# Optimization experiments

Measured on AMD Instinct MI355X. Metric: run time of the kernel, lower is better.

The kernel has to match this reference:

```python
import jax, jax.numpy as jnp
import numpy as np

EPS = 1e-5   # torch F.layer_norm default eps
TOP_K = 20   # int(3*D^2 / (2*hr*N^2 + 10*D)) for D=768, N=196, hr=1.0
NUM_EXPERTS = 200  # 10 * TOP_K


def setup_inputs() -> dict:
    key = jax.random.key(0)
    ks = jax.random.split(key, 6)
    B, N, D = 32, 196, 768
    E, H = NUM_EXPERTS, 196  # H = int(N * hidden_ratio)
    s = 0.02
    return {
        "x": jax.random.normal(ks[0], (B, N, D), jnp.float32),
        "Wr": jax.random.normal(ks[1], (E, D), jnp.float32) * s,   # router.weight
        "W1": jax.random.normal(ks[2], (E, H, N), jnp.float32) * s,  # fc1.weight per expert
        "b1": jnp.zeros((E, H), jnp.float32),
        "W2": jax.random.normal(ks[3], (E, N, H), jnp.float32) * s,  # fc2.weight per expert
        "b2": jnp.zeros((E, N), jnp.float32),
        "Wo": jax.random.normal(ks[4], (D, D), jnp.float32) * s,     # out_proj.weight
        "bo": jnp.zeros((D,), jnp.float32),
    }


def reference(x, Wr, W1, b1, W2, b2, Wo, bo):
    B, N, D = x.shape
    E = Wr.shape[0]
    K = TOP_K

    # Router: per-sample routing on token-mean features
    logits = x.mean(axis=1) @ Wr.T                      # (B, E)
    probs = jax.nn.softmax(logits, axis=-1)             # (B, E)
    w, idx = jax.lax.top_k(probs, K)                    # (B, K) sorted desc, as torch.topk
    w = w / w.sum(axis=-1, keepdims=True)               # renormalize top-k weights

    # TokenMixer operates in (B, D, N) space: layernorm over tokens (no affine),
    # then fc1 (N->H), gelu(tanh), fc2 (H->N).
    xt = jnp.swapaxes(x, 1, 2)                          # (B, D, N)
    mu = xt.mean(axis=-1, keepdims=True)
    var = xt.var(axis=-1, keepdims=True)                # population var (matches F.layer_norm)
    z = (xt - mu) * jax.lax.rsqrt(var + EPS)            # (B, D, N)

    # Gather each sample's K expert weight matrices and batch the MLPs.
    W1g, b1g = W1[idx], b1[idx]                         # (B,K,H,N), (B,K,H)
    W2g, b2g = W2[idx], b2[idx]                         # (B,K,N,H), (B,K,N)

    h = jnp.einsum('bdn,bkhn->bkdh', z, W1g) + b1g[:, :, None, :]
    a = jax.nn.gelu(h, approximate=True)                # tanh-approx GELU
    o = jnp.einsum('bkdh,bknh->bkdn', a, W2g) + b2g[:, :, None, :]

    # Weighted combine over the K selected experts, back to (B, N, D)
    mix = jnp.einsum('bk,bkdn->bnd', w, o)

    out = mix @ Wo.T + bo                               # out_proj

    # Load-balancing aux loss (top-1 assignment fraction vs mean router prob)
    top1 = jax.nn.one_hot(idx[:, 0], E, dtype=probs.dtype)   # (B, E)
    aux = E * jnp.sum(probs.mean(axis=0) * top1.mean(axis=0))
    return out, aux
```

## Files before the change

kernel.cpp:

```cpp
#include <hip/hip_runtime.h>
#include <math.h>

constexpr int B  = 32;
constexpr int N  = 196;
constexpr int D  = 768;
constexpr int E  = 200;
constexpr int TK = 20;

constexpr int NGRP = 4;
constexpr int PRB  = 14336;
constexpr int EXB  = 114688;
constexpr int LK   = 40;

typedef __bf16 bf16x8 __attribute__((ext_vector_type(8)));
typedef __bf16 bf16x4 __attribute__((ext_vector_type(4)));
typedef float  f32x4  __attribute__((ext_vector_type(4)));
typedef long   longx2 __attribute__((ext_vector_type(2)));
typedef unsigned char uchar;

#define GLDS16(gp, lp)                                                        \
  __builtin_amdgcn_global_load_lds(                                           \
      (const __attribute__((address_space(1))) void*)(gp),                    \
      (__attribute__((address_space(3))) void*)(lp), 16, 0, 0)

#define WAITVM12  __builtin_amdgcn_s_waitcnt(0x0F7C)
#define WAITVM8   __builtin_amdgcn_s_waitcnt(0x0F78)
#define WAITVM0   __builtin_amdgcn_s_waitcnt(0x0F70)
#define WAITLGKM0 __builtin_amdgcn_s_waitcnt(0xC07F)
#define BAR       __builtin_amdgcn_s_barrier()

#define KEEP64(v) asm volatile("" : : "v"(v))

__device__ __forceinline__ float gelu_fast(float x) {
  float u = x * fmaf(x * x, 0.044715f, 1.0f);
  float e = exp2f(-2.3022084f * u);
  return x * __builtin_amdgcn_rcpf(1.0f + e);
}

__device__ __forceinline__ uchar f32_to_f8(float v) {
  return (uchar)(__builtin_amdgcn_cvt_pk_fp8_f32(v, v, 0, false) & 0xff);
}

__global__ __launch_bounds__(256) void k_ln(const float* __restrict__ x,
                                            uchar* __restrict__ zb,
                                            float* __restrict__ mu) {
  int b = blockIdx.x / 12, dt = blockIdx.x % 12;
  int d0 = dt * 64;
  int t = threadIdx.x;
  int q = t >> 6, d = t & 63;
  __shared__ float ps[256], pq[256];
  __shared__ float ms[64], rss[64];
  __shared__ alignas(16) uchar zt[64 * 256];

  for (int i = t; i < 1024; i += 256) ((uint4*)zt)[i] = (uint4){0, 0, 0, 0};

  const float* xp = x + ((size_t)b * N + q * 49) * D + d0 + d;
  float v[49];
  float s = 0.f, sq = 0.f;
  #pragma unroll
  for (int n = 0; n < 49; ++n) {
    v[n] = xp[(size_t)n * D];
    s += v[n]; sq += v[n] * v[n];
  }
  ps[t] = s; pq[t] = sq;
  __syncthreads();
  if (t < 64) {
    float S = ps[t] + ps[t + 64] + ps[t + 128] + ps[t + 192];
    float Q = pq[t] + pq[t + 64] + pq[t + 128] + pq[t + 192];
    float m = S * (1.0f / N);
    float var = Q * (1.0f / N) - m * m;
    ms[t] = m; rss[t] = rsqrtf(var + 1e-5f);
    mu[(size_t)b * D + d0 + t] = m;
  }
  __syncthreads();
  float m = ms[d], r = rss[d];
  int dsw = (d >> 1) & 3;
  #pragma unroll
  for (int n = 0; n < 49; ++n) {
    int tok = q * 49 + n;
    int qp = ((tok >> 3) & 3) ^ dsw;
    int off = d * 256 + (tok >> 6) * 64 + qp * 16 + ((tok >> 5) & 1) * 8 + (tok & 7);
    zt[off] = f32_to_f8((v[n] - m) * r);
  }
  __syncthreads();
  #pragma unroll
  for (int pair = 0; pair < 4; ++pair) {
    uint4* dst = (uint4*)(zb + (((size_t)b * 4 + pair) * 768 + d0) * 64);
    dst[t] = ((const uint4*)zt)[(t >> 2) * 16 + pair * 4 + (t & 3)];
  }
}

__global__ __launch_bounds__(256) void k_prep(
    const float* __restrict__ W1, const float* __restrict__ W2,
    const float* __restrict__ Wo,
    uchar* __restrict__ Wf, __bf16* __restrict__ Wob,
    const float* __restrict__ mu, const float* __restrict__ Wr,
    float* __restrict__ probs, int* __restrict__ idxg,
    float* __restrict__ wg) {
  int bx = blockIdx.x;
  int t = threadIdx.x;
  __shared__ alignas(16) uchar ls[112 * 256];
  __shared__ float sp[E];
  __shared__ float smax, ssum;
  __shared__ float svals[TK];
  __shared__ int   sidx[TK];

  if (bx >= 1376) {
    int b = bx - 1376;
    int lane = t & 63, wave = t >> 6;
    float* smu = (float*)ls;
    for (int i = t; i < 768; i += 256) smu[i] = mu[(size_t)b * D + i];
    __syncthreads();
    const float4* m4 = (const float4*)smu;
    #pragma unroll 1
    for (int i = 0; i < 50; ++i) {
      int e = wave * 50 + i;
      const float4* wr4 = (const float4*)(Wr + (size_t)e * D);
      float acc = 0.f;
      #pragma unroll
      for (int j = 0; j < 3; ++j) {
        float4 w = wr4[lane + j * 64], mm = m4[lane + j * 64];
        acc = fmaf(w.x, mm.x, acc); acc = fmaf(w.y, mm.y, acc);
        acc = fmaf(w.z, mm.z, acc); acc = fmaf(w.w, mm.w, acc);
      }
      #pragma unroll
      for (int off = 32; off > 0; off >>= 1) acc += __shfl_down(acc, off);
      if (lane == 0) sp[e] = acc;
    }
    __syncthreads();
    if (t < 64) {
      float mx = -1e30f;
      for (int e = t; e < E; e += 64) mx = fmaxf(mx, sp[e]);
      #pragma unroll
      for (int off = 32; off > 0; off >>= 1) mx = fmaxf(mx, __shfl_down(mx, off));
      if (t == 0) smax = mx;
    }
    __syncthreads();
    if (t < E) sp[t] = exp2f((sp[t] - smax) * 1.44269504f);
    __syncthreads();
    if (t < 64) {
      float s = 0.f;
      for (int e = t; e < E; e += 64) s += sp[e];
      #pragma unroll
      for (int off = 32; off > 0; off >>= 1) s += __shfl_down(s, off);
      if (t == 0) ssum = s;
    }
    __syncthreads();
    if (t < E) {
      sp[t] = sp[t] / ssum;
      probs[(size_t)b * E + t] = sp[t];
    }
    __syncthreads();
    for (int k = 0; k < TK; ++k) {
      if (t < 64) {
        float bv = -1e30f; int bi = 0;
        for (int e = t; e < E; e += 64) {
          float v = sp[e];
          if (v > bv) { bv = v; bi = e; }
        }
        #pragma unroll
        for (int off = 32; off > 0; off >>= 1) {
          float ov = __shfl_down(bv, off);
          int   oi = __shfl_down(bi, off);
          if (ov > bv || (ov == bv && oi < bi)) { bv = ov; bi = oi; }
        }
        if (t == 0) {
          svals[k] = bv; sidx[k] = bi;
          sp[bi] = -2e30f;
        }
      }
      __syncthreads();
    }
    if (t == 0) {
      float s = 0.f;
      for (int k = 0; k < TK; ++k) s += svals[k];
      float inv = 1.0f / s;
      for (int k = 0; k < TK; ++k) {
        wg[b * TK + k]   = svals[k] * inv;
        idxg[b * TK + k] = sidx[k];
      }
    }
    return;
  }

  if (bx >= 800) {
    int i = (bx - 800) * 256 + t;
    float4 v = *(const float4*)&Wo[(size_t)i * 4];
    bf16x4 o = {(__bf16)v.x, (__bf16)v.y, (__bf16)v.z, (__bf16)v.w};
    *(bf16x4*)&Wob[(size_t)i * 4] = o;
    return;
  }

  int e = bx >> 2, mat = (bx >> 1) & 1, half = bx & 1;
  int r0 = half * 112;
  int nrows = half ? 84 : 112;
  for (int i = t; i < 1792; i += 256) ((uint4*)ls)[i] = (uint4){0, 0, 0, 0};
  __syncthreads();
  const float* src = (mat ? W2 : W1) + (size_t)e * 196 * 196;
  for (int i = t; i < nrows * 49; i += 256) {
    int rl = i / 49, c4 = (i - rl * 49) * 4;
    float4 v = *(const float4*)&src[(size_t)(r0 + rl) * 196 + c4];
    int lo = __builtin_amdgcn_cvt_pk_fp8_f32(v.x, v.y, 0, false);
    unsigned int pk = (unsigned int)__builtin_amdgcn_cvt_pk_fp8_f32(v.z, v.w, lo, true);
    *(unsigned int*)&ls[rl * 256 + c4] = pk;
  }
  __syncthreads();
  uchar* dst = Wf + (size_t)e * EXB + mat * 4 * PRB;
  for (int s = t; s < 1792; s += 256) {
    int p = s / 448, rem = s - p * 448;
    int cl = rem >> 2, qp = rem & 3;
    int col = r0 + cl;
    int ql = qp ^ ((col >> 1) & 3);
    unsigned long lo = *(const unsigned long*)&ls[cl * 256 + p * 64 + ql * 8];
    unsigned long hi = *(const unsigned long*)&ls[cl * 256 + p * 64 + 32 + ql * 8];
    longx2 o; o[0] = (long)lo; o[1] = (long)hi;
    *(longx2*)&dst[(size_t)(p * 896 + col * 4 + qp) * 16] = o;
  }
}

__global__ __launch_bounds__(256, 2) void k_expert(
    const uchar* __restrict__ zb, const uchar* __restrict__ Wf,
    const float* __restrict__ b1, const float* __restrict__ b2,
    const int* __restrict__ idxg, const float* __restrict__ wg,
    __bf16* __restrict__ mixg) {
  __shared__ alignas(16) uchar pool[75776];
  __shared__ alignas(16) __bf16 b1s[5 * 196];
  __shared__ float bsum_s[196];
  __shared__ int   eidx_s[5];
  __shared__ float w_s[5];
  uchar* zs  = pool;
  uchar* at  = pool + 16384;
  uchar* wsb = pool + 32768;
  __bf16* tb = (__bf16*)pool;

  int xw = blockIdx.x & 7, rr_ = blockIdx.x >> 3;
  int j = rr_ / 12, dt = rr_ - j * 12;
  int gid = j * 8 + xw;
  int g = gid & 3, b = gid >> 2;
  int d0 = dt * 64;

  int t = threadIdx.x;
  int lane = t & 63, wave = t >> 6;
  int quad = lane >> 4, l16 = lane & 15;
  int wrow = (wave & 1) * 32;
  int wcol = (wave >> 1) * 112;
  int qp = quad ^ ((l16 >> 1) & 3);

  if (t < 5) {
    eidx_s[t] = idxg[b * TK + g * 5 + t];
    w_s[t]    = wg[b * TK + g * 5 + t];
  }
  for (int i = t; i < 980; i += 256) {
    int kk = i / 196, col = i - kk * 196;
    int ee = idxg[b * TK + g * 5 + kk];
    b1s[i] = (__bf16)b1[ee * 196 + col];
  }
  if (t < 196) {
    float s = 0.f;
    #pragma unroll
    for (int k5 = 0; k5 < 5; ++k5) {
      int ee = idxg[b * TK + g * 5 + k5];
      s += wg[b * TK + g * 5 + k5] * b2[ee * 196 + t];
    }
    bsum_s[t] = s;
  }
  __syncthreads();

  {
    const uchar* zbase = zb + ((size_t)b * 4 * 768 + d0) * 64;
    #pragma unroll
    for (int p = 0; p < 4; ++p)
      GLDS16(zbase + (size_t)p * (768 * 64) + t * 16, zs + p * 4096 + t * 16);
  }

  int s0 = t * 16, s1 = (t + 256) * 16, s2 = (t + 512) * 16;
  int s3 = ((t & 127) + 768) * 16;

  auto issue = [&](int qn) {
    int qq = qn > 39 ? 39 : qn;
    int kk2 = qq >> 3, rem = qq & 7;
    const uchar* src = Wf + (size_t)eidx_s[kk2] * EXB + rem * PRB;
    int bi = qn & 3;
    uchar* lb = (bi == 3) ? pool : wsb + bi * PRB;
    GLDS16(src + s0, lb + s0);
    GLDS16(src + s1, lb + s1);
    GLDS16(src + s2, lb + s2);
    GLDS16(src + s3, lb + s3);
  };
  issue(0); issue(1); issue(2);

  WAITVM12;
  BAR;
  const uchar* zbase_l = zs + (wrow + l16) * 64 + qp * 16;
  longx2 zf[3][2];
  #pragma unroll
  for (int p = 0; p < 3; ++p) {
    zf[p][0] = *(const longx2*)(zbase_l + p * 4096);
    zf[p][1] = *(const longx2*)(zbase_l + p * 4096 + 1024);
  }
  long z3r0, z3r1;
  {
    longx2 zt0 = *(const longx2*)(zbase_l + 3 * 4096);
    longx2 zt1 = *(const longx2*)(zbase_l + 3 * 4096 + 1024);
    KEEP64(zt0[1]); KEEP64(zt1[1]);
    z3r0 = zt0[0]; z3r1 = zt1[0];
  }

  const uchar* abase = at + (wrow + l16) * 64 + qp * 16;

  f32x4 macc[14];
  #pragma unroll
  for (int i = 0; i < 14; ++i) macc[i] = (f32x4){0.f, 0.f, 0.f, 0.f};

  #pragma unroll 1
  for (int kk = 0; kk < 5; ++kk) {
    float wkv = w_s[kk];
    f32x4 hacc[14];
    #pragma unroll
    for (int i = 0; i < 14; ++i) hacc[i] = (f32x4){0.f, 0.f, 0.f, 0.f};

    #pragma unroll 1
    for (int p = 0; p < 3; ++p) {
      int q = kk * 8 + p;
      WAITVM8;
      BAR;
      int bi = q & 3;
      const uchar* buf = (bi == 3) ? pool : wsb + bi * PRB;
      const uchar* bb = buf + (wcol + l16) * 64 + qp * 16;
      __builtin_amdgcn_s_setprio(1);
      #pragma unroll
      for (int ct = 0; ct < 7; ++ct) {
        longx2 bf = *(const longx2*)(bb + ct * 1024);
        hacc[ct]     = __builtin_amdgcn_mfma_f32_16x16x32_fp8_fp8(bf[0], zf[p][0][0], hacc[ct], 0, 0, 0);
        hacc[ct]     = __builtin_amdgcn_mfma_f32_16x16x32_fp8_fp8(bf[1], zf[p][0][1], hacc[ct], 0, 0, 0);
        hacc[7 + ct] = __builtin_amdgcn_mfma_f32_16x16x32_fp8_fp8(bf[0], zf[p][1][0], hacc[7 + ct], 0, 0, 0);
        hacc[7 + ct] = __builtin_amdgcn_mfma_f32_16x16x32_fp8_fp8(bf[1], zf[p][1][1], hacc[7 + ct], 0, 0, 0);
      }
      __builtin_amdgcn_s_setprio(0);
      issue(q + 3);
    }
    {
      int q = kk * 8 + 3;
      WAITVM8;
      BAR;
      int bi = q & 3;
      const uchar* buf = (bi == 3) ? pool : wsb + bi * PRB;
      const uchar* bb = buf + (wcol + l16) * 64 + qp * 16;
      __builtin_amdgcn_s_setprio(1);
      #pragma unroll
      for (int ct = 0; ct < 7; ++ct) {
        longx2 bf = *(const longx2*)(bb + ct * 1024);
        KEEP64(bf[1]);
        hacc[ct]     = __builtin_amdgcn_mfma_f32_16x16x32_fp8_fp8(bf[0], z3r0, hacc[ct], 0, 0, 0);
        hacc[7 + ct] = __builtin_amdgcn_mfma_f32_16x16x32_fp8_fp8(bf[0], z3r1, hacc[7 + ct], 0, 0, 0);
      }
      __builtin_amdgcn_s_setprio(0);
      issue(q + 3);
    }

    #pragma unroll
    for (int ct = 0; ct < 7; ++ct) {
      int hb = wcol + ct * 16 + quad * 4;
      bool valid = hb < 196;
      unsigned pk0 = 0u, pk1 = 0u;
      if (valid) {
        bf16x4 b4 = *(const bf16x4*)&b1s[kk * 196 + hb];
        float bv0 = (float)b4[0], bv1 = (float)b4[1];
        float bv2 = (float)b4[2], bv3 = (float)b4[3];
        f32x4 h0 = hacc[ct], h1 = hacc[7 + ct];
        pk0 = (unsigned)__builtin_amdgcn_cvt_pk_fp8_f32(
                  gelu_fast(h0[0] + bv0) * wkv, gelu_fast(h0[1] + bv1) * wkv, 0, false);
        pk0 = (unsigned)__builtin_amdgcn_cvt_pk_fp8_f32(
                  gelu_fast(h0[2] + bv2) * wkv, gelu_fast(h0[3] + bv3) * wkv, (int)pk0, true);
        pk1 = (unsigned)__builtin_amdgcn_cvt_pk_fp8_f32(
                  gelu_fast(h1[0] + bv0) * wkv, gelu_fast(h1[1] + bv1) * wkv, 0, false);
        pk1 = (unsigned)__builtin_amdgcn_cvt_pk_fp8_f32(
                  gelu_fast(h1[2] + bv2) * wkv, gelu_fast(h1[3] + bv3) * wkv, (int)pk1, true);
      }
      int d0r = wrow + l16;
      int addr0 = (hb >> 6) * 4096 + d0r * 64 + ((((hb >> 3) & 3) ^ ((d0r >> 1) & 3)) << 4)
                + ((hb >> 5) & 1) * 8 + (quad & 1) * 4;
      *(unsigned*)&at[addr0]        = pk0;
      *(unsigned*)&at[addr0 + 1024] = pk1;
    }
    WAITLGKM0;

    #pragma unroll 1
    for (int p = 0; p < 3; ++p) {
      int q = kk * 8 + 4 + p;
      WAITVM8;
      BAR;
      int bi = q & 3;
      const uchar* buf = (bi == 3) ? pool : wsb + bi * PRB;
      const uchar* bb = buf + (wcol + l16) * 64 + qp * 16;
      longx2 a0 = *(const longx2*)(abase + p * 4096);
      longx2 a1 = *(const longx2*)(abase + p * 4096 + 1024);
      __builtin_amdgcn_s_setprio(1);
      #pragma unroll
      for (int ct = 0; ct < 7; ++ct) {
        longx2 bf = *(const longx2*)(bb + ct * 1024);
        macc[ct]     = __builtin_amdgcn_mfma_f32_16x16x32_fp8_fp8(a0[0], bf[0], macc[ct], 0, 0, 0);
        macc[ct]     = __builtin_amdgcn_mfma_f32_16x16x32_fp8_fp8(a0[1], bf[1], macc[ct], 0, 0, 0);
        macc[7 + ct] = __builtin_amdgcn_mfma_f32_16x16x32_fp8_fp8(a1[0], bf[0], macc[7 + ct], 0, 0, 0);
        macc[7 + ct] = __builtin_amdgcn_mfma_f32_16x16x32_fp8_fp8(a1[1], bf[1], macc[7 + ct], 0, 0, 0);
      }
      __builtin_amdgcn_s_setprio(0);
      issue(q + 3);
    }
    {
      int q = kk * 8 + 7;
      WAITVM8;
      BAR;
      int bi = q & 3;
      const uchar* buf = (bi == 3) ? pool : wsb + bi * PRB;
      const uchar* bb = buf + (wcol + l16) * 64 + qp * 16;
      long a0h, a1h;
      {
        longx2 at0 = *(const longx2*)(abase + 3 * 4096);
        longx2 at1 = *(const longx2*)(abase + 3 * 4096 + 1024);
        KEEP64(at0[1]); KEEP64(at1[1]);
        a0h = at0[0]; a1h = at1[0];
      }
      __builtin_amdgcn_s_setprio(1);
      #pragma unroll
      for (int ct = 0; ct < 7; ++ct) {
        longx2 bf = *(const longx2*)(bb + ct * 1024);
        KEEP64(bf[1]);
        macc[ct]     = __builtin_amdgcn_mfma_f32_16x16x32_fp8_fp8(a0h, bf[0], macc[ct], 0, 0, 0);
        macc[7 + ct] = __builtin_amdgcn_mfma_f32_16x16x32_fp8_fp8(a1h, bf[0], macc[7 + ct], 0, 0, 0);
      }
      __builtin_amdgcn_s_setprio(0);
      issue(q + 3);
    }
  }

  WAITVM0;
  BAR;
  #pragma unroll
  for (int ct = 0; ct < 7; ++ct) {
    int ncol = wcol + ct * 16 + l16;
    float bsum = (ncol < 196) ? bsum_s[ncol] : 0.f;
    #pragma unroll
    for (int rt = 0; rt < 2; ++rt) {
      f32x4 v = macc[rt * 7 + ct];
      bf16x4 o = {(__bf16)(v[0] + bsum), (__bf16)(v[1] + bsum),
                  (__bf16)(v[2] + bsum), (__bf16)(v[3] + bsum)};
      *(bf16x4*)&tb[ncol * 68 + wrow + rt * 16 + quad * 4] = o;
    }
  }
  __syncthreads();
  __bf16* mp = mixg + ((size_t)(g * B + b) * N) * D + d0;
  #pragma unroll
  for (int i = 0; i < 7; ++i) {
    int s = i * 256 + t;
    if (s < 1568) {
      int n = s >> 3, c = s & 7;
      const uint2* pa = (const uint2*)&tb[n * 68 + c * 8];
      uint2 v0 = pa[0], v1 = pa[1];
      uint4 v = {v0.x, v0.y, v1.x, v1.y};
      *(uint4*)&mp[(size_t)n * D + c * 8] = v;
    }
  }
}

__global__ __launch_bounds__(256, 4) void k_outproj(
    const __bf16* __restrict__ mixg, const __bf16* __restrict__ Wob,
    const float* __restrict__ bo, const float* __restrict__ probs,
    const int* __restrict__ idxg, float* __restrict__ out,
    float* __restrict__ out_aux) {
  __shared__ alignas(16) __bf16 As[32 * LK];
  __shared__ alignas(16) __bf16 Bs[256 * LK];
  const size_t GS = (size_t)B * N * D;

  int t = threadIdx.x;
  if (blockIdx.x == 0 && t < 32) {
    int top1 = idxg[t * TK];
    float s = 0.f;
    for (int bb = 0; bb < B; ++bb) s += probs[(size_t)bb * E + top1];
    #pragma unroll
    for (int off = 16; off > 0; off >>= 1) s += __shfl_down(s, off);
    if (t == 0) out_aux[0] = s * ((float)E / ((float)B * (float)B));
  }

  int m0 = (blockIdx.x % 196) * 32;
  int e0 = (blockIdx.x / 196) * 256;
  int lane = t & 63, wave = t >> 6;
  int quad = lane >> 4, l16 = lane & 15;
  int wrow = (wave & 1) * 16;
  int wcol = (wave >> 1) * 128;
  int arow = t >> 2, ach = t & 3;
  const __bf16* ap0 = mixg + (size_t)(m0 + (arow & 31)) * D + ach * 8;

  f32x4 acc[8];
  #pragma unroll
  for (int i = 0; i < 8; ++i) acc[i] = (f32x4){0.f, 0.f, 0.f, 0.f};

  const uint4* wsrc = (const uint4*)Wob;
  #pragma unroll 1
  for (int c = 0; c < 24; ++c) {
    int k0 = c * 32;
    __syncthreads();
    if (t < 128) {
      const __bf16* ap = ap0 + k0;
      bf16x8 g0 = *(const bf16x8*)(ap);
      bf16x8 g1 = *(const bf16x8*)(ap + GS);
      bf16x8 g2 = *(const bf16x8*)(ap + 2 * GS);
      bf16x8 g3 = *(const bf16x8*)(ap + 3 * GS);
      bf16x8 r;
      #pragma unroll
      for (int jj = 0; jj < 8; ++jj)
        r[jj] = (__bf16)((float)g0[jj] + (float)g1[jj] + (float)g2[jj] + (float)g3[jj]);
      *(bf16x8*)&As[arow * LK + ach * 8] = r;
    }
    for (int p = t; p < 1024; p += 256) {
      int rr = p >> 2, sub = p & 3;
      uint4 v = wsrc[(((size_t)(e0 + rr)) * D + k0) / 8 + sub];
      *(uint4*)&Bs[rr * LK + sub * 8] = v;
    }
    __syncthreads();
    bf16x8 a0 = *(const bf16x8*)&As[(wrow + l16) * LK + quad * 8];
    #pragma unroll
    for (int ct = 0; ct < 8; ++ct) {
      bf16x8 bfr = *(const bf16x8*)&Bs[(wcol + ct * 16 + l16) * LK + quad * 8];
      acc[ct] = __builtin_amdgcn_mfma_f32_16x16x32_bf16(a0, bfr, acc[ct], 0, 0, 0);
    }
  }

  #pragma unroll
  for (int ct = 0; ct < 8; ++ct) {
    int e = e0 + wcol + ct * 16 + l16;
    float bov = bo[e];
    #pragma unroll
    for (int rx = 0; rx < 4; ++rx) {
      int m = m0 + wrow + quad * 4 + rx;
      out[(size_t)m * D + e] = acc[ct][rx] + bov;
    }
  }
}

extern "C" void kernel_launch(void* const* d_in, const int* in_sizes, int n_in,
                              void* d_out, int out_size, void* d_ws, size_t ws_size,
                              hipStream_t stream) {
  const float* x  = (const float*)d_in[0];
  const float* Wr = (const float*)d_in[1];
  const float* W1 = (const float*)d_in[2];
  const float* b1 = (const float*)d_in[3];
  const float* W2 = (const float*)d_in[4];
  const float* b2 = (const float*)d_in[5];
  const float* Wo = (const float*)d_in[6];
  const float* bo = (const float*)d_in[7];
  float* out = (float*)d_out;

  char* p = (char*)d_ws;
  auto alloc = [&](size_t bytes) {
    char* r = p;
    p += (bytes + 255) & ~(size_t)255;
    return r;
  };
  uchar*  zb   = (uchar*)alloc((size_t)B * 4 * 768 * 64);
  float*  mu   = (float*)alloc((size_t)B * D * 4);
  uchar*  Wf   = (uchar*)alloc((size_t)E * EXB);
  __bf16* Wob  = (__bf16*)alloc((size_t)D * D * 2);
  __bf16* mixg = (__bf16*)alloc((size_t)NGRP * B * N * D * 2);
  float*  probs= (float*)alloc((size_t)B * E * 4);
  int*    idxg = (int*)alloc((size_t)B * TK * 4);
  float*  wg   = (float*)alloc((size_t)B * TK * 4);

  k_ln<<<dim3(B * 12), dim3(256), 0, stream>>>(x, zb, mu);
  k_prep<<<dim3(1408), dim3(256), 0, stream>>>(W1, W2, Wo, Wf, Wob,
                                               mu, Wr, probs, idxg, wg);
  k_expert<<<dim3(1536), dim3(256), 0, stream>>>(zb, Wf, b1, b2, idxg, wg, mixg);
  k_outproj<<<dim3(588), dim3(256), 0, stream>>>(mixg, Wob, bo, probs, idxg,
                                                 out, out + (size_t)B * N * D);
}
```

Before: 349.7 us.

## Fuse layernorm into prep kernel and skip padded MFMA column tiles

The separate layernorm launch is merged into the prep kernel as an extra block range. The router blocks now compute the token mean directly from x instead of reading mu from the layernorm output, which removes the dependency between the two. In the expert kernel, waves whose column range starts at 112 skip the seventh 16-column tile, which lies entirely in padding past 196 columns, so those MFMAs and LDS reads are no longer issued. This saves one launch and some wasted compute, but the router blocks now redundantly re-read x, and the uneven per-wave work may affect scheduling.

```diff
diff --git a/kernel.cpp b/kernel.cpp
--- a/kernel.cpp
+++ b/kernel.cpp
@@ -41,75 +41,36 @@
   return (uchar)(__builtin_amdgcn_cvt_pk_fp8_f32(v, v, 0, false) & 0xff);
 }
 
-__global__ __launch_bounds__(256) void k_ln(const float* __restrict__ x,
-                                            uchar* __restrict__ zb,
-                                            float* __restrict__ mu) {
-  int b = blockIdx.x / 12, dt = blockIdx.x % 12;
-  int d0 = dt * 64;
-  int t = threadIdx.x;
-  int q = t >> 6, d = t & 63;
-  __shared__ float ps[256], pq[256];
-  __shared__ float ms[64], rss[64];
-  __shared__ alignas(16) uchar zt[64 * 256];
-
-  for (int i = t; i < 1024; i += 256) ((uint4*)zt)[i] = (uint4){0, 0, 0, 0};
-
-  const float* xp = x + ((size_t)b * N + q * 49) * D + d0 + d;
-  float v[49];
-  float s = 0.f, sq = 0.f;
-  #pragma unroll
-  for (int n = 0; n < 49; ++n) {
-    v[n] = xp[(size_t)n * D];
-    s += v[n]; sq += v[n] * v[n];
-  }
-  ps[t] = s; pq[t] = sq;
-  __syncthreads();
-  if (t < 64) {
-    float S = ps[t] + ps[t + 64] + ps[t + 128] + ps[t + 192];
-    float Q = pq[t] + pq[t + 64] + pq[t + 128] + pq[t + 192];
-    float m = S * (1.0f / N);
-    float var = Q * (1.0f / N) - m * m;
-    ms[t] = m; rss[t] = rsqrtf(var + 1e-5f);
-    mu[(size_t)b * D + d0 + t] = m;
-  }
-  __syncthreads();
-  float m = ms[d], r = rss[d];
-  int dsw = (d >> 1) & 3;
-  #pragma unroll
-  for (int n = 0; n < 49; ++n) {
-    int tok = q * 49 + n;
-    int qp = ((tok >> 3) & 3) ^ dsw;
-    int off = d * 256 + (tok >> 6) * 64 + qp * 16 + ((tok >> 5) & 1) * 8 + (tok & 7);
-    zt[off] = f32_to_f8((v[n] - m) * r);
-  }
-  __syncthreads();
-  #pragma unroll
-  for (int pair = 0; pair < 4; ++pair) {
-    uint4* dst = (uint4*)(zb + (((size_t)b * 4 + pair) * 768 + d0) * 64);
-    dst[t] = ((const uint4*)zt)[(t >> 2) * 16 + pair * 4 + (t & 3)];
-  }
-}
-
 __global__ __launch_bounds__(256) void k_prep(
+    const float* __restrict__ x,
     const float* __restrict__ W1, const float* __restrict__ W2,
-    const float* __restrict__ Wo,
-    uchar* __restrict__ Wf, __bf16* __restrict__ Wob,
-    const float* __restrict__ mu, const float* __restrict__ Wr,
+    const float* __restrict__ Wo, const float* __restrict__ Wr,
+    uchar* __restrict__ zb, uchar* __restrict__ Wf, __bf16* __restrict__ Wob,
     float* __restrict__ probs, int* __restrict__ idxg,
     float* __restrict__ wg) {
   int bx = blockIdx.x;
   int t = threadIdx.x;
-  __shared__ alignas(16) uchar ls[112 * 256];
+  __shared__ alignas(16) uchar ls[28672];
   __shared__ float sp[E];
   __shared__ float smax, ssum;
   __shared__ float svals[TK];
   __shared__ int   sidx[TK];
 
-  if (bx >= 1376) {
-    int b = bx - 1376;
+  if (bx < 32) {
+    int b = bx;
     int lane = t & 63, wave = t >> 6;
     float* smu = (float*)ls;
-    for (int i = t; i < 768; i += 256) smu[i] = mu[(size_t)b * D + i];
+    {
+      const float* xb = x + (size_t)b * N * D;
+      float a0 = 0.f, a1 = 0.f, a2 = 0.f;
+      #pragma unroll 4
+      for (int n = 0; n < 196; ++n) {
+        const float* rp = xb + (size_t)n * D + t;
+        a0 += rp[0]; a1 += rp[256]; a2 += rp[512];
+      }
+      const float inv = 1.0f / (float)N;
+      smu[t] = a0 * inv; smu[t + 256] = a1 * inv; smu[t + 512] = a2 * inv;
+    }
     __syncthreads();
     const float4* m4 = (const float4*)smu;
     #pragma unroll 1
@@ -183,39 +144,89 @@
     return;
   }
 
-  if (bx >= 800) {
-    int i = (bx - 800) * 256 + t;
-    float4 v = *(const float4*)&Wo[(size_t)i * 4];
-    bf16x4 o = {(__bf16)v.x, (__bf16)v.y, (__bf16)v.z, (__bf16)v.w};
-    *(bf16x4*)&Wob[(size_t)i * 4] = o;
+  if (bx < 832) {
+    int bc = bx - 32;
+    int e = bc >> 2, mat = (bc >> 1) & 1, half = bc & 1;
+    int r0 = half * 112;
+    int nrows = half ? 84 : 112;
+    for (int i = t; i < 1792; i += 256) ((uint4*)ls)[i] = (uint4){0, 0, 0, 0};
+    __syncthreads();
+    const float* src = (mat ? W2 : W1) + (size_t)e * 196 * 196;
+    for (int i = t; i < nrows * 49; i += 256) {
+      int rl = i / 49, c4 = (i - rl * 49) * 4;
+      float4 v = *(const float4*)&src[(size_t)(r0 + rl) * 196 + c4];
+      int lo = __builtin_amdgcn_cvt_pk_fp8_f32(v.x, v.y, 0, false);
+      unsigned int pk = (unsigned int)__builtin_amdgcn_cvt_pk_fp8_f32(v.z, v.w, lo, true);
+      *(unsigned int*)&ls[rl * 256 + c4] = pk;
+    }
+    __syncthreads();
+    uchar* dst = Wf + (size_t)e * EXB + mat * 4 * PRB;
+    for (int s = t; s < 1792; s += 256) {
+      int p = s / 448, rem = s - p * 448;
+      int cl = rem >> 2, qp = rem & 3;
+      int col = r0 + cl;
+      int ql = qp ^ ((col >> 1) & 3);
+      unsigned long lo = *(const unsigned long*)&ls[cl * 256 + p * 64 + ql * 8];
+      unsigned long hi = *(const unsigned long*)&ls[cl * 256 + p * 64 + 32 + ql * 8];
+      longx2 o; o[0] = (long)lo; o[1] = (long)hi;
+      *(longx2*)&dst[(size_t)(p * 896 + col * 4 + qp) * 16] = o;
+    }
     return;
   }
 
-  int e = bx >> 2, mat = (bx >> 1) & 1, half = bx & 1;
-  int r0 = half * 112;
-  int nrows = half ? 84 : 112;
-  for (int i = t; i < 1792; i += 256) ((uint4*)ls)[i] = (uint4){0, 0, 0, 0};
-  __syncthreads();
-  const float* src = (mat ? W2 : W1) + (size_t)e * 196 * 196;
-  for (int i = t; i < nrows * 49; i += 256) {
-    int rl = i / 49, c4 = (i - rl * 49) * 4;
-    float4 v = *(const float4*)&src[(size_t)(r0 + rl) * 196 + c4];
-    int lo = __builtin_amdgcn_cvt_pk_fp8_f32(v.x, v.y, 0, false);
-    unsigned int pk = (unsigned int)__builtin_amdgcn_cvt_pk_fp8_f32(v.z, v.w, lo, true);
-    *(unsigned int*)&ls[rl * 256 + c4] = pk;
-  }
-  __syncthreads();
-  uchar* dst = Wf + (size_t)e * EXB + mat * 4 * PRB;
-  for (int s = t; s < 1792; s += 256) {
-    int p = s / 448, rem = s - p * 448;
-    int cl = rem >> 2, qp = rem & 3;
-    int col = r0 + cl;
-    int ql = qp ^ ((col >> 1) & 3);
-    unsigned long lo = *(const unsigned long*)&ls[cl * 256 + p * 64 + ql * 8];
-    unsigned long hi = *(const unsigned long*)&ls[cl * 256 + p * 64 + 32 + ql * 8];
-    longx2 o; o[0] = (long)lo; o[1] = (long)hi;
-    *(longx2*)&dst[(size_t)(p * 896 + col * 4 + qp) * 16] = o;
-  }
+  if (bx < 1216) {
+    int bl = bx - 832;
+    int b = bl / 12, dt = bl % 12;
+    int d0 = dt * 64;
+    int q = t >> 6, d = t & 63;
+    uchar* zt = ls;
+    float* ps = (float*)(ls + 16384);
+    float* pq = (float*)(ls + 17408);
+    float* ms = (float*)(ls + 18432);
+    float* rss = (float*)(ls + 18688);
+
+    for (int i = t; i < 1024; i += 256) ((uint4*)zt)[i] = (uint4){0, 0, 0, 0};
+
+    const float* xp = x + ((size_t)b * N + q * 49) * D + d0 + d;
+    float v[49];
+    float s = 0.f, sq = 0.f;
+    #pragma unroll
+    for (int n = 0; n < 49; ++n) {
+      v[n] = xp[(size_t)n * D];
+      s += v[n]; sq += v[n] * v[n];
+    }
+    ps[t] = s; pq[t] = sq;
+    __syncthreads();
+    if (t < 64) {
+      float S = ps[t] + ps[t + 64] + ps[t + 128] + ps[t + 192];
+      float Q = pq[t] + pq[t + 64] + pq[t + 128] + pq[t + 192];
+      float m = S * (1.0f / N);
+      float var = Q * (1.0f / N) - m * m;
+      ms[t] = m; rss[t] = rsqrtf(var + 1e-5f);
+    }
+    __syncthreads();
+    float m = ms[d], r = rss[d];
+    int dsw = (d >> 1) & 3;
+    #pragma unroll
+    for (int n = 0; n < 49; ++n) {
+      int tok = q * 49 + n;
+      int qp = ((tok >> 3) & 3) ^ dsw;
+      int off = d * 256 + (tok >> 6) * 64 + qp * 16 + ((tok >> 5) & 1) * 8 + (tok & 7);
+      zt[off] = f32_to_f8((v[n] - m) * r);
+    }
+    __syncthreads();
+    #pragma unroll
+    for (int pair = 0; pair < 4; ++pair) {
+      uint4* dst = (uint4*)(zb + (((size_t)b * 4 + pair) * 768 + d0) * 64);
+      dst[t] = ((const uint4*)zt)[(t >> 2) * 16 + pair * 4 + (t & 3)];
+    }
+    return;
+  }
+
+  int i = (bx - 1216) * 256 + t;
+  float4 v = *(const float4*)&Wo[(size_t)i * 4];
+  bf16x4 o = {(__bf16)v.x, (__bf16)v.y, (__bf16)v.z, (__bf16)v.w};
+  *(bf16x4*)&Wob[(size_t)i * 4] = o;
 }
 
 __global__ __launch_bounds__(256, 2) void k_expert(
@@ -244,6 +255,7 @@
   int quad = lane >> 4, l16 = lane & 15;
   int wrow = (wave & 1) * 32;
   int wcol = (wave >> 1) * 112;
+  bool w0 = (wcol == 0);
   int qp = quad ^ ((l16 >> 1) & 3);
 
   if (t < 5) {
@@ -330,11 +342,13 @@
       __builtin_amdgcn_s_setprio(1);
       #pragma unroll
       for (int ct = 0; ct < 7; ++ct) {
-        longx2 bf = *(const longx2*)(bb + ct * 1024);
-        hacc[ct]     = __builtin_amdgcn_mfma_f32_16x16x32_fp8_fp8(bf[0], zf[p][0][0], hacc[ct], 0, 0, 0);
-        hacc[ct]     = __builtin_amdgcn_mfma_f32_16x16x32_fp8_fp8(bf[1], zf[p][0][1], hacc[ct], 0, 0, 0);
-        hacc[7 + ct] = __builtin_amdgcn_mfma_f32_16x16x32_fp8_fp8(bf[0], zf[p][1][0], hacc[7 + ct], 0, 0, 0);
-        hacc[7 + ct] = __builtin_amdgcn_mfma_f32_16x16x32_fp8_fp8(bf[1], zf[p][1][1], hacc[7 + ct], 0, 0, 0);
+        if (ct < 6 || w0) {
+          longx2 bf = *(const longx2*)(bb + ct * 1024);
+          hacc[ct]     = __builtin_amdgcn_mfma_f32_16x16x32_fp8_fp8(bf[0], zf[p][0][0], hacc[ct], 0, 0, 0);
+          hacc[ct]     = __builtin_amdgcn_mfma_f32_16x16x32_fp8_fp8(bf[1], zf[p][0][1], hacc[ct], 0, 0, 0);
+          hacc[7 + ct] = __builtin_amdgcn_mfma_f32_16x16x32_fp8_fp8(bf[0], zf[p][1][0], hacc[7 + ct], 0, 0, 0);
+          hacc[7 + ct] = __builtin_amdgcn_mfma_f32_16x16x32_fp8_fp8(bf[1], zf[p][1][1], hacc[7 + ct], 0, 0, 0);
+        }
       }
       __builtin_amdgcn_s_setprio(0);
       issue(q + 3);
@@ -349,10 +363,12 @@
       __builtin_amdgcn_s_setprio(1);
       #pragma unroll
       for (int ct = 0; ct < 7; ++ct) {
-        longx2 bf = *(const longx2*)(bb + ct * 1024);
-        KEEP64(bf[1]);
-        hacc[ct]     = __builtin_amdgcn_mfma_f32_16x16x32_fp8_fp8(bf[0], z3r0, hacc[ct], 0, 0, 0);
-        hacc[7 + ct] = __builtin_amdgcn_mfma_f32_16x16x32_fp8_fp8(bf[0], z3r1, hacc[7 + ct], 0, 0, 0);
+        if (ct < 6 || w0) {
+          longx2 bf = *(const longx2*)(bb + ct * 1024);
+          KEEP64(bf[1]);
+          hacc[ct]     = __builtin_amdgcn_mfma_f32_16x16x32_fp8_fp8(bf[0], z3r0, hacc[ct], 0, 0, 0);
+          hacc[7 + ct] = __builtin_amdgcn_mfma_f32_16x16x32_fp8_fp8(bf[0], z3r1, hacc[7 + ct], 0, 0, 0);
+        }
       }
       __builtin_amdgcn_s_setprio(0);
       issue(q + 3);
@@ -398,11 +414,13 @@
       __builtin_amdgcn_s_setprio(1);
       #pragma unroll
       for (int ct = 0; ct < 7; ++ct) {
-        longx2 bf = *(const longx2*)(bb + ct * 1024);
-        macc[ct]     = __builtin_amdgcn_mfma_f32_16x16x32_fp8_fp8(a0[0], bf[0], macc[ct], 0, 0, 0);
-        macc[ct]     = __builtin_amdgcn_mfma_f32_16x16x32_fp8_fp8(a0[1], bf[1], macc[ct], 0, 0, 0);
-        macc[7 + ct] = __builtin_amdgcn_mfma_f32_16x16x32_fp8_fp8(a1[0], bf[0], macc[7 + ct], 0, 0, 0);
-        macc[7 + ct] = __builtin_amdgcn_mfma_f32_16x16x32_fp8_fp8(a1[1], bf[1], macc[7 + ct], 0, 0, 0);
+        if (ct < 6 || w0) {
+          longx2 bf = *(const longx2*)(bb + ct * 1024);
+          macc[ct]     = __builtin_amdgcn_mfma_f32_16x16x32_fp8_fp8(a0[0], bf[0], macc[ct], 0, 0, 0);
+          macc[ct]     = __builtin_amdgcn_mfma_f32_16x16x32_fp8_fp8(a0[1], bf[1], macc[ct], 0, 0, 0);
+          macc[7 + ct] = __builtin_amdgcn_mfma_f32_16x16x32_fp8_fp8(a1[0], bf[0], macc[7 + ct], 0, 0, 0);
+          macc[7 + ct] = __builtin_amdgcn_mfma_f32_16x16x32_fp8_fp8(a1[1], bf[1], macc[7 + ct], 0, 0, 0);
+        }
       }
       __builtin_amdgcn_s_setprio(0);
       issue(q + 3);
@@ -424,10 +442,12 @@
       __builtin_amdgcn_s_setprio(1);
       #pragma unroll
       for (int ct = 0; ct < 7; ++ct) {
-        longx2 bf = *(const longx2*)(bb + ct * 1024);
-        KEEP64(bf[1]);
-        macc[ct]     = __builtin_amdgcn_mfma_f32_16x16x32_fp8_fp8(a0h, bf[0], macc[ct], 0, 0, 0);
-        macc[7 + ct] = __builtin_amdgcn_mfma_f32_16x16x32_fp8_fp8(a1h, bf[0], macc[7 + ct], 0, 0, 0);
+        if (ct < 6 || w0) {
+          longx2 bf = *(const longx2*)(bb + ct * 1024);
+          KEEP64(bf[1]);
+          macc[ct]     = __builtin_amdgcn_mfma_f32_16x16x32_fp8_fp8(a0h, bf[0], macc[ct], 0, 0, 0);
+          macc[7 + ct] = __builtin_amdgcn_mfma_f32_16x16x32_fp8_fp8(a1h, bf[0], macc[7 + ct], 0, 0, 0);
+        }
       }
       __builtin_amdgcn_s_setprio(0);
       issue(q + 3);
@@ -558,7 +578,6 @@
     return r;
   };
   uchar*  zb   = (uchar*)alloc((size_t)B * 4 * 768 * 64);
-  float*  mu   = (float*)alloc((size_t)B * D * 4);
   uchar*  Wf   = (uchar*)alloc((size_t)E * EXB);
   __bf16* Wob  = (__bf16*)alloc((size_t)D * D * 2);
   __bf16* mixg = (__bf16*)alloc((size_t)NGRP * B * N * D * 2);
@@ -566,9 +585,8 @@
   int*    idxg = (int*)alloc((size_t)B * TK * 4);
   float*  wg   = (float*)alloc((size_t)B * TK * 4);
 
-  k_ln<<<dim3(B * 12), dim3(256), 0, stream>>>(x, zb, mu);
-  k_prep<<<dim3(1408), dim3(256), 0, stream>>>(W1, W2, Wo, Wf, Wob,
-                                               mu, Wr, probs, idxg, wg);
+  k_prep<<<dim3(1792), dim3(256), 0, stream>>>(x, W1, W2, Wo, Wr,
+                                               zb, Wf, Wob, probs, idxg, wg);
   k_expert<<<dim3(1536), dim3(256), 0, stream>>>(zb, Wf, b1, b2, idxg, wg, mixg);
   k_outproj<<<dim3(588), dim3(256), 0, stream>>>(mixg, Wob, bo, probs, idxg,
                                                  out, out + (size_t)B * N * D);
```

New measurement: 362.5 us. 3.7% more time.
